# Optimization experiments

Hardware: AMD Instinct MI355X
Metric: run time of the kernel (lower is better)

Reference implementation:

```python
import jax, jax.numpy as jnp
import numpy as np
import math

D_MODEL = 1024
N_HEADS = 16
HEAD_DIM = D_MODEL // N_HEADS  # 64
R = HEAD_DIM // 2              # 32
ROPE_BASE = 10000.0
B, T = 4, 2048


def setup_inputs() -> dict:
    key = jax.random.key(0)
    k1, k2, k3, k4, k5 = jax.random.split(key, 5)
    x = jax.random.normal(k1, (B, T, D_MODEL), dtype=jnp.float32)
    Wqkv = jax.random.normal(k2, (3 * D_MODEL, D_MODEL), dtype=jnp.float32) * (1.0 / math.sqrt(D_MODEL))
    Wout = jax.random.normal(k3, (D_MODEL, D_MODEL), dtype=jnp.float32) * (1.0 / math.sqrt(D_MODEL))
    alpha = jax.random.normal(k4, (N_HEADS, R), dtype=jnp.float32) * 0.01
    beta = jax.random.normal(k5, (N_HEADS, R), dtype=jnp.float32) * 0.01
    return {"x": x, "Wqkv": Wqkv, "Wout": Wout, "alpha": alpha, "beta": beta}


def _fourier_bias(alpha, beta, t):
    # omega[r] = base^{-2r/head_dim}, same geometric spacing as RoPE
    omega = ROPE_BASE ** (-2.0 * jnp.arange(R, dtype=jnp.float32) / HEAD_DIM)
    # bias depends only on displacement i-j in [-(t-1), t-1]: compute once per
    # displacement, then gather into the (t, t) matrix (same math as full T x T).
    disp = jnp.arange(-(t - 1), t, dtype=jnp.float32)            # (2t-1,)
    angles = omega[:, None] * disp[None, :]                       # (R, 2t-1)
    vec = jnp.einsum('hr,rk->hk', alpha, jnp.cos(angles)) \
        + jnp.einsum('hr,rk->hk', beta, jnp.sin(angles))          # (H, 2t-1)
    i = jnp.arange(t)
    idx = i[:, None] - i[None, :] + (t - 1)                       # (t, t), delta[i,j]=i-j
    return vec[:, idx]                                            # (H, t, t)


def reference(x, Wqkv, Wout, alpha, beta):
    b, t, d = x.shape
    qkv = x @ Wqkv.T                                              # (B, T, 3D)
    q, k, v = jnp.split(qkv, 3, axis=-1)
    def heads(a):
        return a.reshape(b, t, N_HEADS, HEAD_DIM).transpose(0, 2, 1, 3)  # (B,H,T,dh)
    q, k, v = heads(q), heads(k), heads(v)
    scale = 1.0 / math.sqrt(HEAD_DIM)
    logits = jnp.einsum('bhqd,bhkd->bhqk', q, k) * scale          # (B,H,T,T)
    logits = logits + _fourier_bias(alpha, beta, t)[None]
    causal = jnp.tril(jnp.ones((t, t), dtype=bool))
    logits = jnp.where(causal[None, None], logits, -jnp.inf)
    attn = jax.nn.softmax(logits, axis=-1)
    out = jnp.einsum('bhqk,bhkd->bhqd', attn, v)                  # (B,H,T,dh)
    out = out.transpose(0, 2, 1, 3).reshape(b, t, d)
    return out @ Wout.T
```

## Files before the change

### kernel.cpp

```cpp
#include <hip/hip_runtime.h>
#include <cstdint>
#include <cstddef>

typedef _Float16 f16;
typedef f16 f16x8 __attribute__((ext_vector_type(8)));
typedef __fp16 fp16x2 __attribute__((ext_vector_type(2)));
typedef float f32x4 __attribute__((ext_vector_type(4)));
typedef float f32x16 __attribute__((ext_vector_type(16)));
typedef uint32_t u32;


__device__ __forceinline__ void gload16(const void* g, void* l) {
  __builtin_amdgcn_global_load_lds((const __attribute__((address_space(1))) void*)g,
                                   (__attribute__((address_space(3))) void*)l,
                                   16u, 0, 0u);
}

__device__ __forceinline__ u32 pkrtz(float a, float b) {
  union { fp16x2 v; u32 u; } t;
  t.v = __builtin_amdgcn_cvt_pkrtz(a, b);
  return t.u;
}

__device__ __forceinline__ u32 packh2(float a, float b) { return pkrtz(a, b); }

__device__ __forceinline__ float max3f(float a, float b, float c) {
  return fmaxf(fmaxf(a, b), c);
}

__device__ __forceinline__ void pl32swap(u32& a, u32& b) {
  asm volatile("v_permlane32_swap_b32 %0, %1" : "+v"(a), "+v"(b));
}


__device__ __forceinline__ void cvt8(const float* __restrict__ in,
                                     f16* __restrict__ out, int i) {
  float4 a = *(const float4*)(in + i);
  float4 b = *(const float4*)(in + i + 4);
  f16x8 o;
  o[0] = (f16)a.x; o[1] = (f16)a.y; o[2] = (f16)a.z; o[3] = (f16)a.w;
  o[4] = (f16)b.x; o[5] = (f16)b.y; o[6] = (f16)b.z; o[7] = (f16)b.w;
  *(f16x8*)(out + i) = o;
}

__global__ __launch_bounds__(256) void prep(const float* __restrict__ x,
                                            const float* __restrict__ Wqkv,
                                            const float* __restrict__ Wout,
                                            const float* __restrict__ alpha,
                                            const float* __restrict__ beta,
                                            f16* __restrict__ Xh,
                                            f16* __restrict__ Wqkvh,
                                            f16* __restrict__ Wouth,
                                            f16* __restrict__ U,
                                            f16* __restrict__ Wt) {
  int blk = blockIdx.x;
  int tid = threadIdx.x;
  if (blk < 4096) {
    cvt8(x, Xh, (blk * 256 + tid) * 8);
  } else if (blk < 5632) {
    cvt8(Wqkv, Wqkvh, ((blk - 4096) * 256 + tid) * 8);
  } else if (blk < 6144) {
    cvt8(Wout, Wouth, ((blk - 5632) * 256 + tid) * 8);
  } else {
    int idx = (blk - 6144) * 256 + tid;
    int t = idx >> 5, r = idx & 31;
    float w = powf(10000.0f, -(float)r / 32.0f);
    float ang = w * (float)t;
    float c = cosf(ang), s = sinf(ang);
    const float L2E = 1.44269504089f;
    U[t * 64 + 2 * r]     = (f16)(c * L2E);
    U[t * 64 + 2 * r + 1] = (f16)(s * L2E);
    #pragma unroll
    for (int h = 0; h < 16; ++h) {
      float al = alpha[h * 32 + r], be = beta[h * 32 + r];
      Wt[(size_t)(h * 2048 + t) * 64 + 2 * r]     = (f16)(al * c - be * s);
      Wt[(size_t)(h * 2048 + t) * 64 + 2 * r + 1] = (f16)(al * s + be * c);
    }
  }
}


__global__ __launch_bounds__(512, 2) void gemm_qkv(const f16* __restrict__ A,
                                                   const f16* __restrict__ B,
                                                   f16* __restrict__ Q,
                                                   f16* __restrict__ Kh,
                                                   f16* __restrict__ Vt) {
  __shared__ __align__(16) char sm[147456];
  const int K = 1024;
  int tid = threadIdx.x;
  int lane = tid & 63, wid = tid >> 6;
  int bid = blockIdx.x;
  int xcd = bid & 7;
  int id = bid >> 3;
  int ml = id / 24;
  int nn = id % 24;
  int m0 = (xcd * 4 + ml) * 256;
  int n0 = nn * 128;
  int wm = wid >> 1, wn = wid & 1;
  int c = lane & 15, g = lane >> 4;
  int swz = (c & 7) << 4;

  const f16* asrc[4]; int adst[4];
  #pragma unroll
  for (int i = 0; i < 4; ++i) {
    int p = i * 8192 + tid * 16;
    int row = p >> 7;
    int col = (p & 127) ^ ((row & 7) << 4);
    asrc[i] = A + (size_t)(m0 + row) * K + (col >> 1);
    adst[i] = i * 8192 + wid * 1024;
  }
  const f16* bsrc[2]; int bdst[2];
  #pragma unroll
  for (int i = 0; i < 2; ++i) {
    int p = i * 8192 + tid * 16;
    int row = p >> 7;
    int col = (p & 127) ^ ((row & 7) << 4);
    bsrc[i] = B + (size_t)(n0 + row) * K + (col >> 1);
    bdst[i] = i * 8192 + wid * 1024;
  }

  f32x4 acc[4][4] = {};

  #pragma unroll
  for (int i = 0; i < 4; ++i) gload16(asrc[i], sm + adst[i]);
  #pragma unroll
  for (int i = 0; i < 2; ++i) gload16(bsrc[i], sm + 98304 + bdst[i]);
  #pragma unroll
  for (int i = 0; i < 4; ++i) gload16(asrc[i] + 64, sm + 32768 + adst[i]);
  #pragma unroll
  for (int i = 0; i < 2; ++i) gload16(bsrc[i] + 64, sm + 98304 + 16384 + bdst[i]);

  for (int kt = 0; kt < 16; ++kt) {
    if (kt < 15) asm volatile("s_waitcnt vmcnt(6)" ::: "memory");
    else         asm volatile("s_waitcnt vmcnt(0)" ::: "memory");
    __builtin_amdgcn_s_barrier();

    int j = kt % 3;
    char* As = sm + j * 32768;
    char* Bs = sm + 98304 + j * 16384;
    int jn = (kt + 2) % 3;
    char* Ad = sm + jn * 32768;
    char* Bd = sm + 98304 + jn * 16384;
    bool stg = (kt <= 13);

    if (stg) {
      gload16(asrc[0] + (kt + 2) * 64, Ad + adst[0]);
      gload16(asrc[1] + (kt + 2) * 64, Ad + adst[1]);
      gload16(asrc[2] + (kt + 2) * 64, Ad + adst[2]);
    }
    {
      int co = (g * 16) ^ swz;
      f16x8 af[4], bf[4];
      #pragma unroll
      for (int fr = 0; fr < 4; ++fr)
        af[fr] = *(const f16x8*)(As + (wm * 64 + fr * 16 + c) * 128 + co);
      #pragma unroll
      for (int fn = 0; fn < 4; ++fn)
        bf[fn] = *(const f16x8*)(Bs + (wn * 64 + fn * 16 + c) * 128 + co);
      __builtin_amdgcn_s_setprio(1);
      #pragma unroll
      for (int fr = 0; fr < 4; ++fr)
        #pragma unroll
        for (int fn = 0; fn < 4; ++fn)
          acc[fr][fn] = __builtin_amdgcn_mfma_f32_16x16x32_f16(af[fr], bf[fn], acc[fr][fn], 0, 0, 0);
      __builtin_amdgcn_s_setprio(0);
    }
    if (stg) {
      gload16(asrc[3] + (kt + 2) * 64, Ad + adst[3]);
      gload16(bsrc[0] + (kt + 2) * 64, Bd + bdst[0]);
      gload16(bsrc[1] + (kt + 2) * 64, Bd + bdst[1]);
    }
    {
      int co = (64 + g * 16) ^ swz;
      f16x8 af[4], bf[4];
      #pragma unroll
      for (int fr = 0; fr < 4; ++fr)
        af[fr] = *(const f16x8*)(As + (wm * 64 + fr * 16 + c) * 128 + co);
      #pragma unroll
      for (int fn = 0; fn < 4; ++fn)
        bf[fn] = *(const f16x8*)(Bs + (wn * 64 + fn * 16 + c) * 128 + co);
      __builtin_amdgcn_s_setprio(1);
      #pragma unroll
      for (int fr = 0; fr < 4; ++fr)
        #pragma unroll
        for (int fn = 0; fn < 4; ++fn)
          acc[fr][fn] = __builtin_amdgcn_mfma_f32_16x16x32_f16(af[fr], bf[fn], acc[fr][fn], 0, 0, 0);
      __builtin_amdgcn_s_setprio(0);
    }
  }

  int which = n0 >> 10;
  #pragma unroll
  for (int fr = 0; fr < 4; ++fr) {
    int m = m0 + wm * 64 + fr * 16 + g * 4;
    int b = m >> 11, t = m & 2047;
    #pragma unroll
    for (int fn = 0; fn < 4; ++fn) {
      int n = n0 + wn * 64 + fn * 16 + c;
      int nf = n & 1023, hh = nf >> 6, d = nf & 63;
      if (which == 0) {
        #pragma unroll
        for (int r = 0; r < 4; ++r)
          Q[(size_t)((b * 16 + hh) * 2048 + (t + r)) * 64 + d] = (f16)(acc[fr][fn][r] * 0.180336880111f);
      } else if (which == 1) {
        #pragma unroll
        for (int r = 0; r < 4; ++r)
          Kh[(size_t)((b * 16 + hh) * 2048 + (t + r)) * 64 + d] = (f16)acc[fr][fn][r];
      } else {
        uint2 pk;
        pk.x = packh2(acc[fr][fn][0], acc[fr][fn][1]);
        pk.y = packh2(acc[fr][fn][2], acc[fr][fn][3]);
        *(uint2*)(Vt + (size_t)((b * 16 + hh) * 64 + d) * 2048 + t) = pk;
      }
    }
  }
}


__global__ __launch_bounds__(512, 2) void gemm_out(const f16* __restrict__ A,
                                                   const f16* __restrict__ B,
                                                   float* __restrict__ Cout) {
  __shared__ __align__(16) char sm[147456];
  const int K = 1024;
  int tid = threadIdx.x;
  int lane = tid & 63, wid = tid >> 6;
  int bid = blockIdx.x;
  int xcd = bid & 7;
  int id = bid >> 3;
  int m0 = (xcd * 4 + id / 8) * 256;
  int n0 = (id & 7) * 128;
  int wm = wid >> 1, wn = wid & 1;
  int c = lane & 15, g = lane >> 4;
  int swz = (c & 7) << 4;

  const f16* asrc[4]; int adst[4];
  #pragma unroll
  for (int i = 0; i < 4; ++i) {
    int p = i * 8192 + tid * 16;
    int row = p >> 7;
    int col = (p & 127) ^ ((row & 7) << 4);
    asrc[i] = A + (size_t)(m0 + row) * K + (col >> 1);
    adst[i] = i * 8192 + wid * 1024;
  }
  const f16* bsrc[2]; int bdst[2];
  #pragma unroll
  for (int i = 0; i < 2; ++i) {
    int p = i * 8192 + tid * 16;
    int row = p >> 7;
    int col = (p & 127) ^ ((row & 7) << 4);
    bsrc[i] = B + (size_t)(n0 + row) * K + (col >> 1);
    bdst[i] = i * 8192 + wid * 1024;
  }

  f32x4 acc[4][4] = {};

  #pragma unroll
  for (int i = 0; i < 4; ++i) gload16(asrc[i], sm + adst[i]);
  #pragma unroll
  for (int i = 0; i < 2; ++i) gload16(bsrc[i], sm + 98304 + bdst[i]);
  #pragma unroll
  for (int i = 0; i < 4; ++i) gload16(asrc[i] + 64, sm + 32768 + adst[i]);
  #pragma unroll
  for (int i = 0; i < 2; ++i) gload16(bsrc[i] + 64, sm + 98304 + 16384 + bdst[i]);

  for (int kt = 0; kt < 16; ++kt) {
    if (kt < 15) asm volatile("s_waitcnt vmcnt(6)" ::: "memory");
    else         asm volatile("s_waitcnt vmcnt(0)" ::: "memory");
    __builtin_amdgcn_s_barrier();

    int j = kt % 3;
    char* As = sm + j * 32768;
    char* Bs = sm + 98304 + j * 16384;
    int jn = (kt + 2) % 3;
    char* Ad = sm + jn * 32768;
    char* Bd = sm + 98304 + jn * 16384;
    bool stg = (kt <= 13);

    if (stg) {
      gload16(asrc[0] + (kt + 2) * 64, Ad + adst[0]);
      gload16(asrc[1] + (kt + 2) * 64, Ad + adst[1]);
      gload16(asrc[2] + (kt + 2) * 64, Ad + adst[2]);
    }
    {
      int co = (g * 16) ^ swz;
      f16x8 af[4], bf[4];
      #pragma unroll
      for (int fr = 0; fr < 4; ++fr)
        af[fr] = *(const f16x8*)(As + (wm * 64 + fr * 16 + c) * 128 + co);
      #pragma unroll
      for (int fn = 0; fn < 4; ++fn)
        bf[fn] = *(const f16x8*)(Bs + (wn * 64 + fn * 16 + c) * 128 + co);
      __builtin_amdgcn_s_setprio(1);
      #pragma unroll
      for (int fr = 0; fr < 4; ++fr)
        #pragma unroll
        for (int fn = 0; fn < 4; ++fn)
          acc[fr][fn] = __builtin_amdgcn_mfma_f32_16x16x32_f16(af[fr], bf[fn], acc[fr][fn], 0, 0, 0);
      __builtin_amdgcn_s_setprio(0);
    }
    if (stg) {
      gload16(asrc[3] + (kt + 2) * 64, Ad + adst[3]);
      gload16(bsrc[0] + (kt + 2) * 64, Bd + bdst[0]);
      gload16(bsrc[1] + (kt + 2) * 64, Bd + bdst[1]);
    }
    {
      int co = (64 + g * 16) ^ swz;
      f16x8 af[4], bf[4];
      #pragma unroll
      for (int fr = 0; fr < 4; ++fr)
        af[fr] = *(const f16x8*)(As + (wm * 64 + fr * 16 + c) * 128 + co);
      #pragma unroll
      for (int fn = 0; fn < 4; ++fn)
        bf[fn] = *(const f16x8*)(Bs + (wn * 64 + fn * 16 + c) * 128 + co);
      __builtin_amdgcn_s_setprio(1);
      #pragma unroll
      for (int fr = 0; fr < 4; ++fr)
        #pragma unroll
        for (int fn = 0; fn < 4; ++fn)
          acc[fr][fn] = __builtin_amdgcn_mfma_f32_16x16x32_f16(af[fr], bf[fn], acc[fr][fn], 0, 0, 0);
      __builtin_amdgcn_s_setprio(0);
    }
  }

  #pragma unroll
  for (int fr = 0; fr < 4; ++fr) {
    int m = m0 + wm * 64 + fr * 16 + g * 4;
    #pragma unroll
    for (int fn = 0; fn < 4; ++fn) {
      int n = n0 + wn * 64 + fn * 16 + c;
      #pragma unroll
      for (int r = 0; r < 4; ++r)
        Cout[(size_t)(m + r) * 1024 + n] = acc[fr][fn][r];
    }
  }
}


__global__ __launch_bounds__(256, 3) void attn(const f16* __restrict__ Q,
                                               const f16* __restrict__ Kh,
                                               const f16* __restrict__ Vt,
                                               const f16* __restrict__ U,
                                               const f16* __restrict__ Wt,
                                               f16* __restrict__ AO) {
  __shared__ __align__(16) char sm[49152];
  int tid = threadIdx.x, lane = tid & 63, wid = tid >> 6;
  int l31 = lane & 31, hi = lane >> 5;
  int o = blockIdx.x;
  int qt = 15 - (o >> 6);
  int bh = o & 63;
  int h = bh & 15, b = bh >> 4;
  int swzK = (lane & 15) << 4;
  int swzV = (lane & 7) << 4;

  const f16* ksrc[4]; int kdst[4];
  #pragma unroll
  for (int i = 0; i < 4; ++i) {
    int p = i * 4096 + tid * 16;
    int row = p >> 8;
    int col = (p & 255) ^ ((row & 15) << 4);
    int ce = col >> 1;
    ksrc[i] = (ce < 64) ? (Kh + (size_t)(bh * 2048 + row) * 64 + ce)
                        : (Wt + (size_t)(h * 2048 + row) * 64 + (ce - 64));
    kdst[i] = i * 4096 + wid * 1024;
  }
  const f16* vsrc[2]; int vdst[2];
  #pragma unroll
  for (int i = 0; i < 2; ++i) {
    int p = i * 4096 + tid * 16;
    int row = p >> 7;
    int col = (p & 127) ^ ((row & 7) << 4);
    vsrc[i] = Vt + (size_t)(bh * 64 + row) * 2048 + (col >> 1);
    vdst[i] = i * 4096 + wid * 1024;
  }

  int qrow = qt * 128 + wid * 32 + l31;
  int ktmax = 2 * qt + 1;

  f16x8 qf[8];
  {
    const f16* qp = Q + (size_t)(bh * 2048 + qrow) * 64 + hi * 8;
    const f16* up = U + (size_t)qrow * 64 + hi * 8;
    #pragma unroll
    for (int ks = 0; ks < 4; ++ks) {
      qf[ks]     = *(const f16x8*)(qp + ks * 16);
      qf[4 + ks] = *(const f16x8*)(up + ks * 16);
    }
  }

  float m_i = -1e30f, l_i = 0.0f;
  f32x16 accA = {}, accB = {};

  #pragma unroll
  for (int i = 0; i < 4; ++i) gload16(ksrc[i], sm + kdst[i]);
  #pragma unroll
  for (int i = 0; i < 2; ++i) gload16(vsrc[i], sm + 32768 + vdst[i]);
  __syncthreads();

  for (int kt = 0; kt <= ktmax; ++kt) {
    int cur = kt & 1;
    char* Ks = sm + cur * 16384;
    char* Vs = sm + 32768 + cur * 8192;

    if (kt < ktmax) {
      char* kb = sm + (cur ^ 1) * 16384;
      char* vb = sm + 32768 + (cur ^ 1) * 8192;
      #pragma unroll
      for (int i = 0; i < 4; ++i) gload16(ksrc[i] + (size_t)(kt + 1) * 4096, kb + kdst[i]);
      #pragma unroll
      for (int i = 0; i < 2; ++i) gload16(vsrc[i] + (size_t)(kt + 1) * 64, vb + vdst[i]);
    }

    f32x16 st0 = {}, st1 = {};
    __builtin_amdgcn_s_setprio(1);
    #pragma unroll
    for (int ks = 0; ks < 8; ++ks) {
      int co = (ks * 32 + hi * 16) ^ swzK;
      f16x8 k0 = *(const f16x8*)(Ks + l31 * 256 + co);
      f16x8 k1 = *(const f16x8*)(Ks + (32 + l31) * 256 + co);
      st0 = __builtin_amdgcn_mfma_f32_32x32x16_f16(k0, qf[ks], st0, 0, 0, 0);
      st1 = __builtin_amdgcn_mfma_f32_32x32x16_f16(k1, qf[ks], st1, 0, 0, 0);
    }
    __builtin_amdgcn_s_setprio(0);

    int kv0 = kt * 64;
    if (kv0 + 63 > qt * 128 + wid * 32) {
      #pragma unroll
      for (int r = 0; r < 16; ++r) {
        int kvl = kv0 + (r & 3) + 8 * (r >> 2) + 4 * hi;
        if (kvl > qrow) st0[r] = -1e30f;
        if (kvl + 32 > qrow) st1[r] = -1e30f;
      }
    }

    float pm = fmaxf(st0[0], st1[0]);
    #pragma unroll
    for (int r = 1; r < 16; ++r) pm = max3f(pm, st0[r], st1[r]);
    pm = fmaxf(pm, __shfl_xor(pm, 32, 64));
    if (!__all(pm <= m_i + 8.0f)) {
      float mnew = fmaxf(m_i, pm);
      float sc = __builtin_amdgcn_exp2f(m_i - mnew);
      l_i *= sc;
      accA *= sc;
      accB *= sc;
      m_i = mnew;
    }

    float ps = 0.0f;
    u32 pk0[8], pk1[8];
    #pragma unroll
    for (int j = 0; j < 8; ++j) {
      float a0 = __builtin_amdgcn_exp2f(st0[2 * j] - m_i);
      float a1 = __builtin_amdgcn_exp2f(st0[2 * j + 1] - m_i);
      float b0 = __builtin_amdgcn_exp2f(st1[2 * j] - m_i);
      float b1 = __builtin_amdgcn_exp2f(st1[2 * j + 1] - m_i);
      ps += (a0 + a1) + (b0 + b1);
      pk0[j] = pkrtz(a0, a1);
      pk1[j] = pkrtz(b0, b1);
    }
    ps += __shfl_xor(ps, 32, 64);
    l_i += ps;

    pl32swap(pk0[0], pk0[2]); pl32swap(pk0[1], pk0[3]);
    pl32swap(pk0[4], pk0[6]); pl32swap(pk0[5], pk0[7]);
    pl32swap(pk1[0], pk1[2]); pl32swap(pk1[1], pk1[3]);
    pl32swap(pk1[4], pk1[6]); pl32swap(pk1[5], pk1[7]);

    __builtin_amdgcn_s_setprio(1);
    #pragma unroll
    for (int kb = 0; kb < 4; ++kb) {
      union { u32 w[4]; f16x8 v; } bf;
      const u32* pk = (kb < 2) ? pk0 : pk1;
      int base = (kb & 1) * 4;
      bf.w[0] = pk[base + 0]; bf.w[1] = pk[base + 1];
      bf.w[2] = pk[base + 2]; bf.w[3] = pk[base + 3];
      int co = (kb * 32 + hi * 16) ^ swzV;
      f16x8 v0 = *(const f16x8*)(Vs + l31 * 128 + co);
      f16x8 v1 = *(const f16x8*)(Vs + (32 + l31) * 128 + co);
      accA = __builtin_amdgcn_mfma_f32_32x32x16_f16(v0, bf.v, accA, 0, 0, 0);
      accB = __builtin_amdgcn_mfma_f32_32x32x16_f16(v1, bf.v, accB, 0, 0, 0);
    }
    __builtin_amdgcn_s_setprio(0);
    __syncthreads();
  }

  float inv = __builtin_amdgcn_rcpf(l_i);
  f16* aop = AO + (size_t)(b * 2048 + qrow) * 1024 + h * 64;
  #pragma unroll
  for (int u = 0; u < 4; ++u) {
    uint2 ov;
    ov.x = pkrtz(accA[4 * u] * inv, accA[4 * u + 1] * inv);
    ov.y = pkrtz(accA[4 * u + 2] * inv, accA[4 * u + 3] * inv);
    *(uint2*)(aop + 8 * u + 4 * hi) = ov;
    ov.x = pkrtz(accB[4 * u] * inv, accB[4 * u + 1] * inv);
    ov.y = pkrtz(accB[4 * u + 2] * inv, accB[4 * u + 3] * inv);
    *(uint2*)(aop + 32 + 8 * u + 4 * hi) = ov;
  }
}


extern "C" void kernel_launch(void* const* d_in, const int* in_sizes, int n_in,
                              void* d_out, int out_size, void* d_ws, size_t ws_size,
                              hipStream_t stream) {
  const float* x     = (const float*)d_in[0];
  const float* Wqkv  = (const float*)d_in[1];
  const float* Wout  = (const float*)d_in[2];
  const float* alpha = (const float*)d_in[3];
  const float* beta  = (const float*)d_in[4];

  char* ws = (char*)d_ws;
  f16* Xh    = (f16*)(ws);
  f16* Wqkvh = (f16*)(ws + 16777216);
  f16* Wouth = (f16*)(ws + 23068672);
  f16* Qh    = (f16*)(ws + 25165824);
  f16* Kh    = (f16*)(ws + 41943040);
  f16* Vt    = (f16*)(ws + 58720256);
  f16* U     = (f16*)(ws + 75497472);
  f16* Wt    = (f16*)(ws + 75759616);
  f16* AO    = Xh;

  prep<<<6400, 256, 0, stream>>>(x, Wqkv, Wout, alpha, beta, Xh, Wqkvh, Wouth, U, Wt);
  gemm_qkv<<<768, 512, 0, stream>>>(Xh, Wqkvh, Qh, Kh, Vt);
  attn<<<1024, 256, 0, stream>>>(Qh, Kh, Vt, U, Wt, AO);
  gemm_out<<<256, 512, 0, stream>>>(AO, Wouth, (float*)d_out);
}
```

Baseline: 157.2 us.

## Halve attention KV tile to 32 keys and cut LDS for higher occupancy

```diff
diff --git a/kernel.cpp b/kernel.cpp
--- a/kernel.cpp
+++ b/kernel.cpp
@@ -336,13 +336,13 @@
 }
 
 
-__global__ __launch_bounds__(256, 3) void attn(const f16* __restrict__ Q,
+__global__ __launch_bounds__(256, 4) void attn(const f16* __restrict__ Q,
                                                const f16* __restrict__ Kh,
                                                const f16* __restrict__ Vt,
                                                const f16* __restrict__ U,
                                                const f16* __restrict__ Wt,
                                                f16* __restrict__ AO) {
-  __shared__ __align__(16) char sm[49152];
+  __shared__ __align__(16) char sm[32768];
   int tid = threadIdx.x, lane = tid & 63, wid = tid >> 6;
   int l31 = lane & 31, hi = lane >> 5;
   int o = blockIdx.x;
@@ -352,9 +352,9 @@
   int swzK = (lane & 15) << 4;
   int swzV = (lane & 7) << 4;
 
-  const f16* ksrc[4]; int kdst[4];
-  #pragma unroll
-  for (int i = 0; i < 4; ++i) {
+  const f16* ksrc[2]; int kdst[2];
+  #pragma unroll
+  for (int i = 0; i < 2; ++i) {
     int p = i * 4096 + tid * 16;
     int row = p >> 8;
     int col = (p & 255) ^ ((row & 15) << 4);
@@ -374,7 +374,7 @@
   }
 
   int qrow = qt * 128 + wid * 32 + l31;
-  int ktmax = 2 * qt + 1;
+  int ktmax = 4 * qt + 3;
 
   f16x8 qf[8];
   {
@@ -391,50 +391,52 @@
   f32x16 accA = {}, accB = {};
 
   #pragma unroll
-  for (int i = 0; i < 4; ++i) gload16(ksrc[i], sm + kdst[i]);
-  #pragma unroll
-  for (int i = 0; i < 2; ++i) gload16(vsrc[i], sm + 32768 + vdst[i]);
+  for (int i = 0; i < 2; ++i) gload16(ksrc[i], sm + kdst[i]);
+  #pragma unroll
+  for (int i = 0; i < 2; ++i) gload16(vsrc[i], sm + 16384 + vdst[i]);
   __syncthreads();
 
   for (int kt = 0; kt <= ktmax; ++kt) {
-    int cur = kt & 1;
-    char* Ks = sm + cur * 16384;
-    char* Vs = sm + 32768 + cur * 8192;
-
+    char* Ks = sm + (kt & 1) * 8192;
+    char* Vs = sm + 16384 + ((kt >> 1) & 1) * 8192;
+    int vhalf = (kt & 1) * 64;
+
+    if ((kt & 1) == 0 && kt + 2 <= ktmax) {
+      char* vb = sm + 16384 + (((kt >> 1) & 1) ^ 1) * 8192;
+      #pragma unroll
+      for (int i = 0; i < 2; ++i)
+        gload16(vsrc[i] + (size_t)((kt >> 1) + 1) * 64, vb + vdst[i]);
+    }
     if (kt < ktmax) {
-      char* kb = sm + (cur ^ 1) * 16384;
-      char* vb = sm + 32768 + (cur ^ 1) * 8192;
-      #pragma unroll
-      for (int i = 0; i < 4; ++i) gload16(ksrc[i] + (size_t)(kt + 1) * 4096, kb + kdst[i]);
-      #pragma unroll
-      for (int i = 0; i < 2; ++i) gload16(vsrc[i] + (size_t)(kt + 1) * 64, vb + vdst[i]);
-    }
-
-    f32x16 st0 = {}, st1 = {};
+      char* kb = sm + ((kt + 1) & 1) * 8192;
+      #pragma unroll
+      for (int i = 0; i < 2; ++i)
+        gload16(ksrc[i] + (size_t)(kt + 1) * 2048, kb + kdst[i]);
+    }
+
+    f32x16 st0 = {};
     __builtin_amdgcn_s_setprio(1);
     #pragma unroll
     for (int ks = 0; ks < 8; ++ks) {
       int co = (ks * 32 + hi * 16) ^ swzK;
       f16x8 k0 = *(const f16x8*)(Ks + l31 * 256 + co);
-      f16x8 k1 = *(const f16x8*)(Ks + (32 + l31) * 256 + co);
       st0 = __builtin_amdgcn_mfma_f32_32x32x16_f16(k0, qf[ks], st0, 0, 0, 0);
-      st1 = __builtin_amdgcn_mfma_f32_32x32x16_f16(k1, qf[ks], st1, 0, 0, 0);
     }
     __builtin_amdgcn_s_setprio(0);
 
-    int kv0 = kt * 64;
-    if (kv0 + 63 > qt * 128 + wid * 32) {
+    int kv0 = kt * 32;
+    if (kv0 + 31 > qt * 128 + wid * 32) {
       #pragma unroll
       for (int r = 0; r < 16; ++r) {
         int kvl = kv0 + (r & 3) + 8 * (r >> 2) + 4 * hi;
         if (kvl > qrow) st0[r] = -1e30f;
-        if (kvl + 32 > qrow) st1[r] = -1e30f;
       }
     }
 
-    float pm = fmaxf(st0[0], st1[0]);
-    #pragma unroll
-    for (int r = 1; r < 16; ++r) pm = max3f(pm, st0[r], st1[r]);
+    float pm = st0[0];
+    #pragma unroll
+    for (int r = 1; r < 15; r += 2) pm = max3f(pm, st0[r], st0[r + 1]);
+    pm = fmaxf(pm, st0[15]);
     pm = fmaxf(pm, __shfl_xor(pm, 32, 64));
     if (!__all(pm <= m_i + 8.0f)) {
       float mnew = fmaxf(m_i, pm);
@@ -446,34 +448,28 @@
     }
 
     float ps = 0.0f;
-    u32 pk0[8], pk1[8];
+    u32 pk0[8];
     #pragma unroll
     for (int j = 0; j < 8; ++j) {
       float a0 = __builtin_amdgcn_exp2f(st0[2 * j] - m_i);
       float a1 = __builtin_amdgcn_exp2f(st0[2 * j + 1] - m_i);
-      float b0 = __builtin_amdgcn_exp2f(st1[2 * j] - m_i);
-      float b1 = __builtin_amdgcn_exp2f(st1[2 * j + 1] - m_i);
-      ps += (a0 + a1) + (b0 + b1);
+      ps += (a0 + a1);
       pk0[j] = pkrtz(a0, a1);
-      pk1[j] = pkrtz(b0, b1);
     }
     ps += __shfl_xor(ps, 32, 64);
     l_i += ps;
 
     pl32swap(pk0[0], pk0[2]); pl32swap(pk0[1], pk0[3]);
     pl32swap(pk0[4], pk0[6]); pl32swap(pk0[5], pk0[7]);
-    pl32swap(pk1[0], pk1[2]); pl32swap(pk1[1], pk1[3]);
-    pl32swap(pk1[4], pk1[6]); pl32swap(pk1[5], pk1[7]);
 
     __builtin_amdgcn_s_setprio(1);
     #pragma unroll
-    for (int kb = 0; kb < 4; ++kb) {
+    for (int kb = 0; kb < 2; ++kb) {
       union { u32 w[4]; f16x8 v; } bf;
-      const u32* pk = (kb < 2) ? pk0 : pk1;
-      int base = (kb & 1) * 4;
-      bf.w[0] = pk[base + 0]; bf.w[1] = pk[base + 1];
-      bf.w[2] = pk[base + 2]; bf.w[3] = pk[base + 3];
-      int co = (kb * 32 + hi * 16) ^ swzV;
+      int base = kb * 4;
+      bf.w[0] = pk0[base + 0]; bf.w[1] = pk0[base + 1];
+      bf.w[2] = pk0[base + 2]; bf.w[3] = pk0[base + 3];
+      int co = (vhalf + kb * 32 + hi * 16) ^ swzV;
       f16x8 v0 = *(const f16x8*)(Vs + l31 * 128 + co);
       f16x8 v1 = *(const f16x8*)(Vs + (32 + l31) * 128 + co);
       accA = __builtin_amdgcn_mfma_f32_32x32x16_f16(v0, bf.v, accA, 0, 0, 0);
```

After: 164.4 us. +4.6%, slower.
